# Performance work log

Hardware: AMD Instinct MI355X
Metric: run time of the kernel (lower is better)

Reference implementation:

```python
import jax, jax.numpy as jnp
import numpy as np

N = 100000
E = 1600000
D = 128   # path_code_size
H = 32    # GIN hidden dim (hard-coded in module)
BN_EPS = 1e-5
GIN_EPS = 0.0  # GINConv default eps


def gin_conv(x, src, dst, Wa, ba, Wb, bb, num_nodes):
    # sum-aggregate neighbor features: messages x[src] scattered to dst
    agg = jax.ops.segment_sum(x[src], dst, num_segments=num_nodes)
    h = (1.0 + GIN_EPS) * x + agg
    h = jax.nn.relu(h @ Wa + ba)
    return h @ Wb + bb


def batch_norm(x, gamma, beta):
    # training-mode BN over the node dimension (biased variance, like torch)
    mean = jnp.mean(x, axis=0)
    var = jnp.mean((x - mean) ** 2, axis=0)
    return (x - mean) * jax.lax.rsqrt(var + BN_EPS) * gamma + beta


def setup_inputs() -> dict:
    key = jax.random.key(0)
    ks = jax.random.split(key, 12)
    x = jax.random.normal(ks[0], (N, D), dtype=jnp.float32)
    edge_index = jax.random.randint(ks[1], (2, E), 0, N, dtype=jnp.int64)

    def lin(k, fan_in, fan_out):
        bound = 1.0 / np.sqrt(fan_in)
        kw, kb = jax.random.split(k)
        W = jax.random.uniform(kw, (fan_in, fan_out), jnp.float32, -bound, bound)
        b = jax.random.uniform(kb, (fan_out,), jnp.float32, -bound, bound)
        return W, b

    W1a, b1a = lin(ks[2], D, H)
    W1b, b1b = lin(ks[3], H, H)
    W2a, b2a = lin(ks[4], H, H)
    W2b, b2b = lin(ks[5], H, D)
    return {
        "x": x, "edge_index": edge_index,
        "W1a": W1a, "b1a": b1a, "W1b": W1b, "b1b": b1b,
        "g1": jnp.ones((H,), jnp.float32), "be1": jnp.zeros((H,), jnp.float32),
        "W2a": W2a, "b2a": b2a, "W2b": W2b, "b2b": b2b,
        "g2": jnp.ones((D,), jnp.float32), "be2": jnp.zeros((D,), jnp.float32),
    }


def reference(x, edge_index, W1a, b1a, W1b, b1b, g1, be1, W2a, b2a, W2b, b2b, g2, be2):
    src, dst = edge_index[0], edge_index[1]
    h = jax.nn.relu(gin_conv(x, src, dst, W1a, b1a, W1b, b1b, N))
    h = batch_norm(h, g1, be1)
    h = jax.nn.relu(gin_conv(h, src, dst, W2a, b2a, W2b, b2b, N))
    h = batch_norm(h, g2, be2)
    return h
```

## Files before the change

kernel.cpp:

```cpp
#include <hip/hip_runtime.h>

constexpr int NN  = 100000;
constexpr int NE  = 1600000;
constexpr int D   = 128;
constexpr int H   = 32;
constexpr int CAP = 64;


__global__ __launch_bounds__(256) void k_fill(const int* __restrict__ src,
                                              const int* __restrict__ dst,
                                              int* __restrict__ cnt,
                                              int* __restrict__ slots) {
    for (int e = blockIdx.x * blockDim.x + threadIdx.x; e < NE;
         e += gridDim.x * blockDim.x) {
        const int d = dst[e];
        const int pos = atomicAdd(&cnt[d], 1);
        if (pos < CAP) slots[d * CAP + pos] = src[e];
    }
}

__global__ __launch_bounds__(256) void k_xw1(const float* __restrict__ x,
                                             const float* __restrict__ W,
                                             float* __restrict__ z) {
    __shared__ float Wl[D * H];
    for (int i = threadIdx.x; i < D * H; i += blockDim.x) Wl[i] = W[i];
    __syncthreads();
    const int j = threadIdx.x & 31;
    const int g = threadIdx.x >> 5;
    const int groups = blockDim.x >> 5;
    for (int n = blockIdx.x * groups + g; n < NN; n += gridDim.x * groups) {
        const float* xr = x + (size_t)n * D;
        float acc = 0.f;
#pragma unroll 8
        for (int k = 0; k < D; ++k) acc = fmaf(xr[k], Wl[k * H + j], acc);
        z[n * H + j] = acc;
    }
}

__global__ __launch_bounds__(256) void k_mlp1(const float* __restrict__ z,
                                              const int* __restrict__ cnt,
                                              const int* __restrict__ slots,
                                              const float* __restrict__ b1a,
                                              const float* __restrict__ W1b,
                                              const float* __restrict__ b1b,
                                              float* __restrict__ r1,
                                              float* __restrict__ gsum,
                                              float* __restrict__ gsq) {
    __shared__ float Wl[H * H];
    __shared__ float lsum[H], lsq[H];
    for (int i = threadIdx.x; i < H * H; i += blockDim.x) Wl[i] = W1b[i];
    if (threadIdx.x < H) { lsum[threadIdx.x] = 0.f; lsq[threadIdx.x] = 0.f; }
    __syncthreads();
    const int j = threadIdx.x & 31;
    const int g = threadIdx.x >> 5;
    const int groups = blockDim.x >> 5;
    const float ba = b1a[j], bb = b1b[j];
    float psum = 0.f, psq = 0.f;
    for (int n = blockIdx.x * groups + g; n < NN; n += gridDim.x * groups) {
        float t = z[n * H + j] + ba;
        const int deg = min(cnt[n], CAP);
        const int* row = slots + n * CAP;
        int e = 0;
        for (; e + 8 <= deg; e += 8) {
            const int4 a = *(const int4*)(row + e);
            const int4 b = *(const int4*)(row + e + 4);
            const float t0 = z[a.x * H + j], t1 = z[a.y * H + j];
            const float t2 = z[a.z * H + j], t3 = z[a.w * H + j];
            const float t4 = z[b.x * H + j], t5 = z[b.y * H + j];
            const float t6 = z[b.z * H + j], t7 = z[b.w * H + j];
            t += ((t0 + t1) + (t2 + t3)) + ((t4 + t5) + (t6 + t7));
        }
        for (; e < deg; ++e) t += z[row[e] * H + j];
        t = fmaxf(t, 0.f);
        float u = bb;
#pragma unroll
        for (int k = 0; k < H; ++k) u = fmaf(__shfl(t, k, 32), Wl[k * H + j], u);
        const float r = fmaxf(u, 0.f);
        r1[n * H + j] = r;
        psum += r;
        psq = fmaf(r, r, psq);
    }
    atomicAdd(&lsum[j], psum);
    atomicAdd(&lsq[j], psq);
    __syncthreads();
    if (threadIdx.x < H) {
        atomicAdd(&gsum[threadIdx.x], lsum[threadIdx.x]);
        atomicAdd(&gsq[threadIdx.x], lsq[threadIdx.x]);
    }
}

__global__ void k_finalize(const float* __restrict__ gsum, const float* __restrict__ gsq,
                           const float* __restrict__ gamma, const float* __restrict__ beta,
                           float* __restrict__ scale, float* __restrict__ shift, int C) {
    const int j = threadIdx.x;
    if (j < C) {
        const float mean = gsum[j] * (1.f / NN);
        const float var  = gsq[j] * (1.f / NN) - mean * mean;
        const float sc   = gamma[j] * rsqrtf(var + 1e-5f);
        scale[j] = sc;
        shift[j] = beta[j] - mean * sc;
    }
}

__global__ __launch_bounds__(256) void k_bn_w2a(const float* __restrict__ r1,
                                                const float* __restrict__ scale,
                                                const float* __restrict__ shift,
                                                const float* __restrict__ W2a,
                                                float* __restrict__ z2) {
    __shared__ float Wl[H * H];
    for (int i = threadIdx.x; i < H * H; i += blockDim.x) Wl[i] = W2a[i];
    __syncthreads();
    const int j = threadIdx.x & 31;
    const int g = threadIdx.x >> 5;
    const int groups = blockDim.x >> 5;
    const float sc = scale[j], sh = shift[j];
    for (int n = blockIdx.x * groups + g; n < NN; n += gridDim.x * groups) {
        const float y = fmaf(r1[n * H + j], sc, sh);
        float u = 0.f;
#pragma unroll
        for (int k = 0; k < H; ++k) u = fmaf(__shfl(y, k, 32), Wl[k * H + j], u);
        z2[n * H + j] = u;
    }
}

__global__ __launch_bounds__(256) void k_mlp2(const float* __restrict__ z2,
                                              const int* __restrict__ cnt,
                                              const int* __restrict__ slots,
                                              const float* __restrict__ b2a,
                                              const float* __restrict__ W2b,
                                              const float* __restrict__ b2b,
                                              float* __restrict__ out,
                                              float* __restrict__ gsum,
                                              float* __restrict__ gsq) {
    __shared__ float Wl[H * D];
    __shared__ float lsum[D], lsq[D];
    for (int i = threadIdx.x; i < H * D; i += blockDim.x) Wl[i] = W2b[i];
    if (threadIdx.x < D) { lsum[threadIdx.x] = 0.f; lsq[threadIdx.x] = 0.f; }
    __syncthreads();
    const int lane = threadIdx.x & 63;
    const int wid  = threadIdx.x >> 6;
    const int j    = lane & 31;
    const int half = lane >> 5;
    const float ba  = b2a[j];
    const float bb0 = b2b[lane], bb1 = b2b[64 + lane];
    float ps0 = 0.f, pq0 = 0.f, ps1 = 0.f, pq1 = 0.f;
    const int nw = (gridDim.x * blockDim.x) >> 6;
    for (int n = blockIdx.x * 4 + wid; n < NN; n += nw) {
        const int* row = slots + n * CAP;
        const int deg = min(cnt[n], CAP);
        float tp = (half == 0) ? z2[n * H + j] + ba : 0.f;
        int e = half;
        for (; e + 6 < deg; e += 8) {
            const int s0 = row[e],     s1 = row[e + 2];
            const int s2 = row[e + 4], s3 = row[e + 6];
            const float a0 = z2[s0 * H + j], a1 = z2[s1 * H + j];
            const float a2 = z2[s2 * H + j], a3 = z2[s3 * H + j];
            tp += (a0 + a1) + (a2 + a3);
        }
        for (; e < deg; e += 2) tp += z2[row[e] * H + j];
        float t = tp + __shfl_xor(tp, 32);
        t = fmaxf(t, 0.f);
        float u0 = bb0, u1 = bb1;
#pragma unroll
        for (int k = 0; k < H; ++k) {
            const float tk = __shfl(t, k, 32);
            u0 = fmaf(tk, Wl[k * D + lane], u0);
            u1 = fmaf(tk, Wl[k * D + 64 + lane], u1);
        }
        const float r0 = fmaxf(u0, 0.f), r1v = fmaxf(u1, 0.f);
        out[(size_t)n * D + lane]      = r0;
        out[(size_t)n * D + 64 + lane] = r1v;
        ps0 += r0;  pq0 = fmaf(r0, r0, pq0);
        ps1 += r1v; pq1 = fmaf(r1v, r1v, pq1);
    }
    atomicAdd(&lsum[lane], ps0);      atomicAdd(&lsq[lane], pq0);
    atomicAdd(&lsum[64 + lane], ps1); atomicAdd(&lsq[64 + lane], pq1);
    __syncthreads();
    if (threadIdx.x < D) {
        atomicAdd(&gsum[threadIdx.x], lsum[threadIdx.x]);
        atomicAdd(&gsq[threadIdx.x], lsq[threadIdx.x]);
    }
}

__global__ __launch_bounds__(256) void k_bn_out(float* __restrict__ out,
                                                const float* __restrict__ scale,
                                                const float* __restrict__ shift) {
    const int total = NN * D / 4;
    float4* o4 = (float4*)out;
    for (int i = blockIdx.x * blockDim.x + threadIdx.x; i < total;
         i += gridDim.x * blockDim.x) {
        float4 v = o4[i];
        const int c = (i & 31) * 4;
        v.x = fmaf(v.x, scale[c + 0], shift[c + 0]);
        v.y = fmaf(v.y, scale[c + 1], shift[c + 1]);
        v.z = fmaf(v.z, scale[c + 2], shift[c + 2]);
        v.w = fmaf(v.w, scale[c + 3], shift[c + 3]);
        o4[i] = v;
    }
}

extern "C" void kernel_launch(void* const* d_in, const int* in_sizes, int n_in,
                              void* d_out, int out_size, void* d_ws, size_t ws_size,
                              hipStream_t stream) {
    const float* x   = (const float*)d_in[0];
    const int*   ei  = (const int*)d_in[1];
    const float* W1a = (const float*)d_in[2];
    const float* b1a = (const float*)d_in[3];
    const float* W1b = (const float*)d_in[4];
    const float* b1b = (const float*)d_in[5];
    const float* g1  = (const float*)d_in[6];
    const float* be1 = (const float*)d_in[7];
    const float* W2a = (const float*)d_in[8];
    const float* b2a = (const float*)d_in[9];
    const float* W2b = (const float*)d_in[10];
    const float* b2b = (const float*)d_in[11];
    const float* g2  = (const float*)d_in[12];
    const float* be2 = (const float*)d_in[13];
    float* out = (float*)d_out;
    const int* src = ei;
    const int* dst = ei + NE;

    float* ws = (float*)d_ws;
    float* z   = ws;
    float* r1  = ws + (size_t)NN * H;
    int*   cnt = (int*)(ws + 2 * (size_t)NN * H);
    float* st  = ws + 2 * (size_t)NN * H + NN;
    int*   slots = (int*)(st + 640);
    float* gsum1 = st;        float* gsq1 = st + 32;
    float* sc1   = st + 64;   float* sh1  = st + 96;
    float* gsum2 = st + 128;  float* gsq2 = st + 256;
    float* sc2   = st + 384;  float* sh2  = st + 512;

    hipMemsetAsync(cnt, 0, (NN + 640) * sizeof(float), stream);

    k_fill<<<2048, 256, 0, stream>>>(src, dst, cnt, slots);

    k_xw1<<<2048, 256, 0, stream>>>(x, W1a, z);
    k_mlp1<<<2048, 256, 0, stream>>>(z, cnt, slots, b1a, W1b, b1b, r1, gsum1, gsq1);
    k_finalize<<<1, 128, 0, stream>>>(gsum1, gsq1, g1, be1, sc1, sh1, H);

    k_bn_w2a<<<2048, 256, 0, stream>>>(r1, sc1, sh1, W2a, z);
    k_mlp2<<<2500, 256, 0, stream>>>(z, cnt, slots, b2a, W2b, b2b, out, gsum2, gsq2);
    k_finalize<<<1, 128, 0, stream>>>(gsum2, gsq2, g2, be2, sc2, sh2, D);
    k_bn_out<<<2048, 256, 0, stream>>>(out, sc2, sh2);
}
```

Measured before the change: 587.6 us.

## Split neighbor gather into source-range tiled passes for cache locality

Moves the neighbor aggregation out of the two MLP kernels into a separate gather kernel. The gather runs four times, once per quarter of the source-node range, and accumulates into a buffer. Each pass touches only a 3.2 MB slice of z, so the random gathers should mostly hit in cache. The cost is rereading the slot lists four times, per-edge range checks and branch divergence, and extra accumulate traffic on the agg buffer. The mlp2 grid size also changes.

```diff
diff --git a/kernel.cpp b/kernel.cpp
--- a/kernel.cpp
+++ b/kernel.cpp
@@ -5,6 +5,8 @@
 constexpr int D   = 128;
 constexpr int H   = 32;
 constexpr int CAP = 64;
+constexpr int NTILE = 4;
+constexpr int TILE_SZ = NN / NTILE;
 
 
 __global__ __launch_bounds__(256) void k_fill(const int* __restrict__ src,
@@ -37,13 +39,44 @@
     }
 }
 
+__global__ __launch_bounds__(256) void k_gather(const float* __restrict__ z,
+                                                const int* __restrict__ cnt,
+                                                const int* __restrict__ slots,
+                                                float* __restrict__ agg,
+                                                int lo, int first) {
+    const int j = threadIdx.x & 31;
+    const int g = threadIdx.x >> 5;
+    const int groups = blockDim.x >> 5;
+    for (int n = blockIdx.x * groups + g; n < NN; n += gridDim.x * groups) {
+        const int deg = min(cnt[n], CAP);
+        const int* row = slots + n * CAP;
+        float t = 0.f;
+        for (int e = 0; e < deg; e += 8) {
+            const int4 a = *(const int4*)(row + e);
+            const int4 b = *(const int4*)(row + e + 4);
+            if ((unsigned)(a.x - lo) < (unsigned)TILE_SZ)                 t += z[a.x * H + j];
+            if (e + 1 < deg && (unsigned)(a.y - lo) < (unsigned)TILE_SZ)  t += z[a.y * H + j];
+            if (e + 2 < deg && (unsigned)(a.z - lo) < (unsigned)TILE_SZ)  t += z[a.z * H + j];
+            if (e + 3 < deg && (unsigned)(a.w - lo) < (unsigned)TILE_SZ)  t += z[a.w * H + j];
+            if (e + 4 < deg && (unsigned)(b.x - lo) < (unsigned)TILE_SZ)  t += z[b.x * H + j];
+            if (e + 5 < deg && (unsigned)(b.y - lo) < (unsigned)TILE_SZ)  t += z[b.y * H + j];
+            if (e + 6 < deg && (unsigned)(b.z - lo) < (unsigned)TILE_SZ)  t += z[b.z * H + j];
+            if (e + 7 < deg && (unsigned)(b.w - lo) < (unsigned)TILE_SZ)  t += z[b.w * H + j];
+        }
+        float* ap = agg + (size_t)n * H + j;
+        if (first) {
+            __builtin_nontemporal_store(t, ap);
+        } else {
+            __builtin_nontemporal_store(t + *ap, ap);
+        }
+    }
+}
+
 __global__ __launch_bounds__(256) void k_mlp1(const float* __restrict__ z,
-                                              const int* __restrict__ cnt,
-                                              const int* __restrict__ slots,
+                                              float* __restrict__ buf,
                                               const float* __restrict__ b1a,
                                               const float* __restrict__ W1b,
                                               const float* __restrict__ b1b,
-                                              float* __restrict__ r1,
                                               float* __restrict__ gsum,
                                               float* __restrict__ gsq) {
     __shared__ float Wl[H * H];
@@ -57,26 +90,13 @@
     const float ba = b1a[j], bb = b1b[j];
     float psum = 0.f, psq = 0.f;
     for (int n = blockIdx.x * groups + g; n < NN; n += gridDim.x * groups) {
-        float t = z[n * H + j] + ba;
-        const int deg = min(cnt[n], CAP);
-        const int* row = slots + n * CAP;
-        int e = 0;
-        for (; e + 8 <= deg; e += 8) {
-            const int4 a = *(const int4*)(row + e);
-            const int4 b = *(const int4*)(row + e + 4);
-            const float t0 = z[a.x * H + j], t1 = z[a.y * H + j];
-            const float t2 = z[a.z * H + j], t3 = z[a.w * H + j];
-            const float t4 = z[b.x * H + j], t5 = z[b.y * H + j];
-            const float t6 = z[b.z * H + j], t7 = z[b.w * H + j];
-            t += ((t0 + t1) + (t2 + t3)) + ((t4 + t5) + (t6 + t7));
-        }
-        for (; e < deg; ++e) t += z[row[e] * H + j];
+        float t = z[n * H + j] + buf[n * H + j] + ba;
         t = fmaxf(t, 0.f);
         float u = bb;
 #pragma unroll
         for (int k = 0; k < H; ++k) u = fmaf(__shfl(t, k, 32), Wl[k * H + j], u);
         const float r = fmaxf(u, 0.f);
-        r1[n * H + j] = r;
+        buf[n * H + j] = r;
         psum += r;
         psq = fmaf(r, r, psq);
     }
@@ -124,8 +144,7 @@
 }
 
 __global__ __launch_bounds__(256) void k_mlp2(const float* __restrict__ z2,
-                                              const int* __restrict__ cnt,
-                                              const int* __restrict__ slots,
+                                              const float* __restrict__ agg,
                                               const float* __restrict__ b2a,
                                               const float* __restrict__ W2b,
                                               const float* __restrict__ b2b,
@@ -140,25 +159,12 @@
     const int lane = threadIdx.x & 63;
     const int wid  = threadIdx.x >> 6;
     const int j    = lane & 31;
-    const int half = lane >> 5;
     const float ba  = b2a[j];
     const float bb0 = b2b[lane], bb1 = b2b[64 + lane];
     float ps0 = 0.f, pq0 = 0.f, ps1 = 0.f, pq1 = 0.f;
     const int nw = (gridDim.x * blockDim.x) >> 6;
     for (int n = blockIdx.x * 4 + wid; n < NN; n += nw) {
-        const int* row = slots + n * CAP;
-        const int deg = min(cnt[n], CAP);
-        float tp = (half == 0) ? z2[n * H + j] + ba : 0.f;
-        int e = half;
-        for (; e + 6 < deg; e += 8) {
-            const int s0 = row[e],     s1 = row[e + 2];
-            const int s2 = row[e + 4], s3 = row[e + 6];
-            const float a0 = z2[s0 * H + j], a1 = z2[s1 * H + j];
-            const float a2 = z2[s2 * H + j], a3 = z2[s3 * H + j];
-            tp += (a0 + a1) + (a2 + a3);
-        }
-        for (; e < deg; e += 2) tp += z2[row[e] * H + j];
-        float t = tp + __shfl_xor(tp, 32);
+        float t = z2[(size_t)n * H + j] + agg[(size_t)n * H + j] + ba;
         t = fmaxf(t, 0.f);
         float u0 = bb0, u1 = bb1;
 #pragma unroll
@@ -221,10 +227,10 @@
     const int* dst = ei + NE;
 
     float* ws = (float*)d_ws;
-    float* z   = ws;
-    float* r1  = ws + (size_t)NN * H;
-    int*   cnt = (int*)(ws + 2 * (size_t)NN * H);
-    float* st  = ws + 2 * (size_t)NN * H + NN;
+    float* z    = ws;
+    float* buf  = ws + (size_t)NN * H;
+    int*   cnt  = (int*)(ws + 2 * (size_t)NN * H);
+    float* st   = ws + 2 * (size_t)NN * H + NN;
     int*   slots = (int*)(st + 640);
     float* gsum1 = st;        float* gsq1 = st + 32;
     float* sc1   = st + 64;   float* sh1  = st + 96;
@@ -236,11 +242,15 @@
     k_fill<<<2048, 256, 0, stream>>>(src, dst, cnt, slots);
 
     k_xw1<<<2048, 256, 0, stream>>>(x, W1a, z);
-    k_mlp1<<<2048, 256, 0, stream>>>(z, cnt, slots, b1a, W1b, b1b, r1, gsum1, gsq1);
+    for (int t = 0; t < NTILE; ++t)
+        k_gather<<<2048, 256, 0, stream>>>(z, cnt, slots, buf, t * TILE_SZ, t == 0);
+    k_mlp1<<<2048, 256, 0, stream>>>(z, buf, b1a, W1b, b1b, gsum1, gsq1);
     k_finalize<<<1, 128, 0, stream>>>(gsum1, gsq1, g1, be1, sc1, sh1, H);
 
-    k_bn_w2a<<<2048, 256, 0, stream>>>(r1, sc1, sh1, W2a, z);
-    k_mlp2<<<2500, 256, 0, stream>>>(z, cnt, slots, b2a, W2b, b2b, out, gsum2, gsq2);
+    k_bn_w2a<<<2048, 256, 0, stream>>>(buf, sc1, sh1, W2a, z);
+    for (int t = 0; t < NTILE; ++t)
+        k_gather<<<2048, 256, 0, stream>>>(z, cnt, slots, buf, t * TILE_SZ, t == 0);
+    k_mlp2<<<2048, 256, 0, stream>>>(z, buf, b2a, W2b, b2b, out, gsum2, gsq2);
     k_finalize<<<1, 128, 0, stream>>>(gsum2, gsq2, g2, be2, sc2, sh2, D);
     k_bn_out<<<2048, 256, 0, stream>>>(out, sc2, sh2);
 }
```

After: 702.7 us. 1.2x slower.
